# Performance work log

Measured on AMD Instinct MI355X. Metric: run time of the kernel, lower is better.

Reference implementation:

```python
import jax, jax.numpy as jnp
import numpy as np

B, T, D, H = 64, 512, 512, 128

def swish(x):
    return x * jax.nn.sigmoid(x)

def setup_inputs() -> dict:
    key = jax.random.key(0)
    ks = jax.random.split(key, 8)
    X = jax.random.normal(ks[0], (B, T, D), dtype=jnp.float32)
    # strictly-upper-triangular random binary adjacency -> valid DAG
    adj = jax.random.bernoulli(ks[1], 0.3, (T, T)).astype(jnp.float32)
    dag = jnp.triu(adj, k=1)
    s = 1.0 / np.sqrt(D)
    Wk = jax.random.normal(ks[2], (H, D), dtype=jnp.float32) * s
    bk = jax.random.normal(ks[3], (H,), dtype=jnp.float32) * 0.01
    Wq = jax.random.normal(ks[4], (H, D), dtype=jnp.float32) * s
    bq = jax.random.normal(ks[5], (H,), dtype=jnp.float32) * 0.01
    Wv = jax.random.normal(ks[6], (H, D), dtype=jnp.float32) * s
    bv = jax.random.normal(ks[7], (H,), dtype=jnp.float32) * 0.01
    return {"X": X, "dag": dag, "Wk": Wk, "bk": bk, "Wq": Wq, "bq": bq, "Wv": Wv, "bv": bv}

def reference(X, dag, Wk, bk, Wq, bq, Wv, bv):
    K = swish(jnp.einsum('btd,hd->bth', X, Wk) + bk)  # [B,T,H]
    Q = swish(jnp.einsum('btd,hd->bth', X, Wq) + bq)
    V = swish(jnp.einsum('btd,hd->bth', X, Wv) + bv)
    S_qk = jnp.einsum('bqh,bkh->bqk', Q, K) / jnp.sqrt(jnp.float32(H))  # [B,T,T]
    dagT = dag.T  # [T,T]
    Sprime = dagT * jnp.einsum('ij,bjk->bik', dagT, S_qk)  # [B,T,T]
    # masked_fill(Sprime == 0, -inf) then softmax; rows that are all -inf
    # would produce NaN in torch and are replaced by zeros -> do it nan-free.
    nz = Sprime != 0
    masked = jnp.where(nz, Sprime, -jnp.inf)
    row_valid = jnp.any(nz, axis=-1, keepdims=True)  # [B,T,1]
    masked_safe = jnp.where(row_valid, masked, 0.0)
    probs = jax.nn.softmax(masked_safe, axis=-1) * row_valid  # [B,T,T]
    Vprime = jnp.einsum('ij,bjh->bih', dagT, V)  # [B,T,H]
    O = jnp.einsum('bqk,bkh->bqh', probs, V) + Vprime
    return O
```

## Files before the change

kernel.cpp:

```cpp
#include <hip/hip_runtime.h>
#include <hip/hip_bf16.h>

#define Bn 64
#define Tn 512
#define Dn 512
#define Hn 128
#define BT (Bn*Tn)

typedef unsigned short u16;
typedef unsigned long long u64;
typedef __attribute__((ext_vector_type(8))) short bf16x8;
typedef __attribute__((ext_vector_type(4))) float f32x4;

__device__ __forceinline__ u16 f2bf(float f) {
  union { float f; unsigned u; } v; v.f = f;
  unsigned r = (v.u + 0x7FFFu + ((v.u >> 16) & 1u)) >> 16;
  return (u16)r;
}

__device__ __forceinline__ bf16x8 pack8(float4 a, float4 b) {
  bf16x8 o;
  o[0] = (short)f2bf(a.x); o[1] = (short)f2bf(a.y);
  o[2] = (short)f2bf(a.z); o[3] = (short)f2bf(a.w);
  o[4] = (short)f2bf(b.x); o[5] = (short)f2bf(b.y);
  o[6] = (short)f2bf(b.z); o[7] = (short)f2bf(b.w);
  return o;
}

__device__ __forceinline__ void gload16(const void* g, void* lds) {
  __builtin_amdgcn_global_load_lds(
      (const __attribute__((address_space(1))) unsigned int*)g,
      (__attribute__((address_space(3))) unsigned int*)lds, 16, 0, 0);
}

__global__ __launch_bounds__(256) void conv_w3(const float4* __restrict__ Wk,
                                               const float4* __restrict__ Wq,
                                               const float4* __restrict__ Wv,
                                               ushort4* __restrict__ out) {
  int idx = blockIdx.x * 256 + threadIdx.x;
  int which = idx >> 14, j = idx & 16383;
  const float4* src = (which == 0) ? Wk : (which == 1) ? Wq : Wv;
  float4 v = src[j];
  ushort4 o; o.x = f2bf(v.x); o.y = f2bf(v.y); o.z = f2bf(v.z); o.w = f2bf(v.w);
  out[idx] = o;
}

__global__ __launch_bounds__(256) void dag_tr(const float* __restrict__ dag,
                                              u16* __restrict__ dagT,
                                              u64* __restrict__ bits) {
  __shared__ float s[64][65];
  int bx = blockIdx.x & 7, by = blockIdx.x >> 3;
  int r0 = by * 64, c0 = bx * 64;
  int t = threadIdx.x;
  int c4 = t & 15, rr = t >> 4;
#pragma unroll
  for (int q = 0; q < 4; ++q) {
    int r = rr + q * 16;
    float4 v = *(const float4*)&dag[(size_t)(r0 + r) * Tn + c0 + c4 * 4];
    s[c4 * 4 + 0][r] = v.x; s[c4 * 4 + 1][r] = v.y;
    s[c4 * 4 + 2][r] = v.z; s[c4 * 4 + 3][r] = v.w;
  }
  __syncthreads();
#pragma unroll
  for (int q = 0; q < 4; ++q) {
    int il = rr + q * 16;
    ushort4 o;
    u64 b4 = 0;
#pragma unroll
    for (int r = 0; r < 4; ++r) {
      float v = s[il][c4 * 4 + r];
      ((u16*)&o)[r] = f2bf(v);
      b4 |= (u64)(v != 0.f) << (c4 * 4 + r);
    }
    *(ushort4*)&dagT[(size_t)(c0 + il) * Tn + r0 + c4 * 4] = o;
    b4 |= __shfl_xor(b4, 1, 64);
    b4 |= __shfl_xor(b4, 2, 64);
    b4 |= __shfl_xor(b4, 4, 64);
    b4 |= __shfl_xor(b4, 8, 64);
    if (c4 == 0) bits[(size_t)(c0 + il) * 8 + (r0 >> 6)] = b4;
  }
}

__global__ __launch_bounds__(256, 2) void qkv3(
    const float* __restrict__ X, const u16* __restrict__ Wcat,
    const float* __restrict__ bk, const float* __restrict__ bq,
    const float* __restrict__ bv,
    u16* __restrict__ Kb, u16* __restrict__ QT, u16* __restrict__ VT) {
  __shared__ u16 sm[28672];
  int m0 = blockIdx.x * 64;
  int tid = threadIdx.x, lane = tid & 63, wave = tid >> 6;
  int col0 = lane & 15, rg = lane >> 4, kcb = rg * 16;
  int swl = (col0 & 7) << 4;
  int xrow = tid >> 2, xcq = tid & 3;
  f32x4 acc[3][4][2] = {};
  const char* Wb = (const char*)Wcat;
  char* smb = (char*)sm;

  for (int kt = 0; kt < Dn; kt += 64) {
    {
      const float4* src = (const float4*)(X + (size_t)(m0 + xrow) * Dn + kt + xcq * 16);
      float4 a0 = src[0], a1 = src[1], a2 = src[2], a3 = src[3];
      int sw = (xrow & 7) << 4;
      *(bf16x8*)(smb + xrow * 128 + ((xcq * 32) ^ sw)) = pack8(a0, a1);
      *(bf16x8*)(smb + xrow * 128 + ((xcq * 32 + 16) ^ sw)) = pack8(a2, a3);
    }
#pragma unroll
    for (int q = 0; q < 12; ++q) {
      int c2 = wave * 12 + q;
      int which = c2 >> 4, idx = c2 & 15;
      int flat = idx * 1024 + lane * 16;
      int row = flat >> 7, colb = flat & 127;
      int sw = (row & 7) << 4;
      gload16(Wb + (size_t)which * 131072 + (size_t)row * 1024 + (kt << 1) + (colb ^ sw),
              smb + 8192 + which * 16384 + idx * 1024);
    }
    __syncthreads();
    bf16x8 af[4][2];
#pragma unroll
    for (int m = 0; m < 4; ++m)
#pragma unroll
      for (int kk = 0; kk < 2; ++kk)
        af[m][kk] = *(const bf16x8*)(smb + (m * 16 + col0) * 128 + ((kk * 64 + kcb) ^ swl));
#pragma unroll
    for (int which = 0; which < 3; ++which) {
      bf16x8 bfr[2][2];
#pragma unroll
      for (int n = 0; n < 2; ++n)
#pragma unroll
        for (int kk = 0; kk < 2; ++kk)
          bfr[n][kk] = *(const bf16x8*)(smb + 8192 + which * 16384 +
                                        (wave * 32 + n * 16 + col0) * 128 + ((kk * 64 + kcb) ^ swl));
#pragma unroll
      for (int kk = 0; kk < 2; ++kk)
#pragma unroll
        for (int m = 0; m < 4; ++m)
#pragma unroll
          for (int n = 0; n < 2; ++n)
            acc[which][m][n] = __builtin_amdgcn_mfma_f32_16x16x32_bf16(
                af[m][kk], bfr[n][kk], acc[which][m][n], 0, 0, 0);
    }
    __syncthreads();
  }

  {
#pragma unroll
    for (int n = 0; n < 2; ++n) {
      int nl = wave * 32 + n * 16 + col0;
      float bs = bk[nl];
#pragma unroll
      for (int m = 0; m < 4; ++m)
#pragma unroll
        for (int r = 0; r < 4; ++r) {
          int tl = m * 16 + rg * 4 + r;
          float x = acc[0][m][n][r] + bs;
          *(u16*)(smb + tl * 256 + ((nl * 2) ^ ((tl & 7) << 4))) = f2bf(x / (1.f + __expf(-x)));
        }
    }
    __syncthreads();
#pragma unroll
    for (int p = 0; p < 4; ++p) {
      int c = p * 256 + tid;
      int t = c >> 4, c16 = c & 15;
      bf16x8 v = *(const bf16x8*)(smb + t * 256 + ((c16 * 16) ^ ((t & 7) << 4)));
      *(bf16x8*)&Kb[(size_t)(m0 + t) * Hn + c16 * 8] = v;
    }
  }
  int bb = m0 >> 9, tt0 = m0 & (Tn - 1);
#pragma unroll
  for (int which = 1; which < 3; ++which) {
    const float* bias = (which == 1) ? bq : bv;
    u16* dst = (which == 1) ? QT : VT;
    __syncthreads();
#pragma unroll
    for (int n = 0; n < 2; ++n) {
      int nl = wave * 32 + n * 16 + col0;
      float bs = bias[nl];
#pragma unroll
      for (int m = 0; m < 4; ++m)
#pragma unroll
        for (int r = 0; r < 4; ++r) {
          int tl = m * 16 + rg * 4 + r;
          float x = acc[which][m][n][r] + bs;
          *(u16*)(smb + nl * 128 + ((tl * 2) ^ ((nl & 7) << 4))) = f2bf(x / (1.f + __expf(-x)));
        }
    }
    __syncthreads();
#pragma unroll
    for (int p = 0; p < 4; ++p) {
      int c = p * 256 + tid;
      int h = c >> 3, c8 = c & 7;
      bf16x8 v = *(const bf16x8*)(smb + h * 128 + ((c8 * 16) ^ ((h & 7) << 4)));
      *(bf16x8*)&dst[((size_t)bb * Hn + h) * Tn + tt0 + c8 * 8] = v;
    }
  }
}

__global__ __launch_bounds__(256, 2) void dattn(
    const u16* __restrict__ dagT, const u16* __restrict__ QT,
    const u16* __restrict__ VT, const u16* __restrict__ Kb,
    const u64* __restrict__ dbits, float* __restrict__ O) {
  __shared__ char smA[65536];
  __shared__ u16 smQ2[8192];

  int bid = blockIdx.x;
  int xcd = bid & 7, rst = bid >> 3;
  int bx = rst & 7, b = (rst >> 3) * 8 + xcd;
  int m0 = bx * 64;
  int tid = threadIdx.x, lane = tid & 63, wave = tid >> 6;
  int col0 = lane & 15, g = lane >> 4;
  int swl = (col0 & 7) << 4;

  const char* Ab = (const char*)(dagT + (size_t)m0 * Tn);
  const char* Qb = (const char*)(QT + (size_t)b * Hn * Tn);
  const char* Vb = (const char*)(VT + (size_t)b * Hn * Tn);
  const char* Kb0 = (const char*)(Kb + (size_t)b * Tn * Hn);

  f32x4 accq[4][2] = {};
  f32x4 accv[4][2] = {};
  for (int kt = 0; kt < Tn; kt += 64) {
#pragma unroll
    for (int q = 0; q < 2; ++q) {
      int ch = wave * 2 + q;
      int flat = ch * 1024 + lane * 16;
      int row = flat >> 7, colb = flat & 127;
      int sw = (row & 7) << 4;
      gload16(Ab + (size_t)row * 1024 + kt * 2 + (colb ^ sw), smA + ch * 1024);
    }
#pragma unroll
    for (int q = 0; q < 4; ++q) {
      int ch = wave * 4 + q;
      int flat = ch * 1024 + lane * 16;
      int row = flat >> 7, colb = flat & 127;
      int sw = (row & 7) << 4;
      gload16(Qb + (size_t)row * 1024 + kt * 2 + (colb ^ sw), smA + 8192 + ch * 1024);
      gload16(Vb + (size_t)row * 1024 + kt * 2 + (colb ^ sw), smA + 24576 + ch * 1024);
    }
    __syncthreads();
    bf16x8 af[4][2], fq[2][2], fv[2][2];
#pragma unroll
    for (int m = 0; m < 4; ++m)
#pragma unroll
      for (int kk = 0; kk < 2; ++kk)
        af[m][kk] = *(const bf16x8*)(smA + (m * 16 + col0) * 128 + ((kk * 64 + g * 16) ^ swl));
#pragma unroll
    for (int n = 0; n < 2; ++n)
#pragma unroll
      for (int kk = 0; kk < 2; ++kk) {
        fq[n][kk] = *(const bf16x8*)(smA + 8192 + (wave * 32 + n * 16 + col0) * 128 + ((kk * 64 + g * 16) ^ swl));
        fv[n][kk] = *(const bf16x8*)(smA + 24576 + (wave * 32 + n * 16 + col0) * 128 + ((kk * 64 + g * 16) ^ swl));
      }
#pragma unroll
    for (int kk = 0; kk < 2; ++kk)
#pragma unroll
      for (int m = 0; m < 4; ++m)
#pragma unroll
        for (int n = 0; n < 2; ++n) {
          accq[m][n] = __builtin_amdgcn_mfma_f32_16x16x32_bf16(af[m][kk], fq[n][kk], accq[m][n], 0, 0, 0);
          accv[m][n] = __builtin_amdgcn_mfma_f32_16x16x32_bf16(af[m][kk], fv[n][kk], accv[m][n], 0, 0, 0);
        }
    __syncthreads();
  }

  const float scale = 0.08838834764831845f;
#pragma unroll
  for (int m = 0; m < 4; ++m)
#pragma unroll
    for (int n = 0; n < 2; ++n)
#pragma unroll
      for (int r = 0; r < 4; ++r) {
        int q = m * 16 + g * 4 + r;
        int h = wave * 32 + n * 16 + col0;
        *(u16*)((char*)smQ2 + q * 256 + ((h * 2) ^ ((q & 7) << 4))) = f2bf(accq[m][n][r] * scale);
      }

#define STAGE_K(c_, buf_)                                                      \
  {                                                                            \
    _Pragma("unroll")                                                          \
    for (int q = 0; q < 8; ++q) {                                              \
      int ch = wave * 8 + q;                                                   \
      int flat = ch * 1024 + lane * 16;                                        \
      int row = flat >> 8, colb = flat & 255;                                  \
      gload16(Kb0 + (size_t)((c_) * 128 + row) * 256 + (colb ^ ((row & 7) << 4)), \
              smA + (buf_) * 32768 + ch * 1024);                               \
    }                                                                          \
  }

  STAGE_K(0, 0);
  __syncthreads();

  int qrow = wave * 16 + col0;
  bf16x8 bq[4];
#pragma unroll
  for (int kk = 0; kk < 4; ++kk)
    bq[kk] = *(const bf16x8*)((char*)smQ2 + qrow * 256 + ((kk * 64 + g * 16) ^ ((qrow & 7) << 4)));
  const u64* dbq = dbits + (size_t)(m0 + qrow) * 8;
  u64 md[8];
#pragma unroll
  for (int w = 0; w < 8; ++w) md[w] = dbq[w];

  f32x4 sa[32] = {};
#pragma unroll
  for (int c = 0; c < 4; ++c) {
    if (c < 3) STAGE_K(c + 1, (c + 1) & 1);
    const char* kb = smA + (c & 1) * 32768;
#pragma unroll
    for (int t = 0; t < 8; ++t)
#pragma unroll
      for (int kk = 0; kk < 4; ++kk) {
        bf16x8 ak = *(const bf16x8*)(kb + (t * 16 + col0) * 256 + ((kk * 64 + g * 16) ^ swl));
        sa[c * 8 + t] = __builtin_amdgcn_mfma_f32_16x16x32_bf16(ak, bq[kk], sa[c * 8 + t], 0, 0, 0);
      }
    if (c < 3) __syncthreads();
  }

  float mx = -INFINITY;
#pragma unroll
  for (int t = 0; t < 32; ++t)
#pragma unroll
    for (int r = 0; r < 4; ++r) {
      int k = t * 16 + g * 4 + r;
      float v = ((md[k >> 6] >> (k & 63)) & 1) ? sa[t][r] : -INFINITY;
      sa[t][r] = v;
      mx = fmaxf(mx, v);
    }
  mx = fmaxf(mx, __shfl_xor(mx, 16, 64));
  mx = fmaxf(mx, __shfl_xor(mx, 32, 64));
  float mm = (mx == -INFINITY) ? 0.f : mx;

  ushort4 pk[32];
  float s = 0.f;
#pragma unroll
  for (int t = 0; t < 32; ++t) {
    ushort4 p;
#pragma unroll
    for (int r = 0; r < 4; ++r) {
      float v = sa[t][r];
      float e = (v == -INFINITY) ? 0.f : __expf(v - mm);
      s += e;
      ((u16*)&p)[r] = f2bf(e);
    }
    pk[t] = p;
  }
  s += __shfl_xor(s, 16, 64);
  s += __shfl_xor(s, 32, 64);
  float* linv = (float*)smQ2;
  if (g == 0) linv[qrow] = (s > 0.f) ? (1.f / s) : 0.f;

  char* smP = smA;
  f32x4 acco[4][2] = {};
  int sww = (qrow & 7) << 4;

#pragma unroll
  for (int c = 0; c < 4; ++c) {
    __syncthreads();
#pragma unroll
    for (int tt = 0; tt < 8; ++tt)
      *(ushort4*)(smP + qrow * 256 + ((tt * 32 + g * 8) ^ sww)) = pk[c * 8 + tt];
    __syncthreads();

#pragma unroll
    for (int kk = 0; kk < 4; ++kk) {
      bf16x8 pa[4], vb[2];
#pragma unroll
      for (int m = 0; m < 4; ++m) {
        int row = m * 16 + col0;
        pa[m] = *(const bf16x8*)(smP + row * 256 + ((kk * 64 + g * 16) ^ ((row & 7) << 4)));
      }
#pragma unroll
      for (int n = 0; n < 2; ++n)
        vb[n] = *(const bf16x8*)(Vb + (size_t)(wave * 32 + n * 16 + col0) * 1024 + c * 256 + kk * 64 + g * 16);
#pragma unroll
      for (int m = 0; m < 4; ++m)
#pragma unroll
        for (int n = 0; n < 2; ++n)
          acco[m][n] = __builtin_amdgcn_mfma_f32_16x16x32_bf16(pa[m], vb[n], acco[m][n], 0, 0, 0);
    }
  }

#pragma unroll
  for (int m = 0; m < 4; ++m)
#pragma unroll
    for (int r = 0; r < 4; ++r) {
      int ql = m * 16 + g * 4 + r;
      float inv = linv[ql];
      int i = m0 + ql;
#pragma unroll
      for (int n = 0; n < 2; ++n) {
        int h = wave * 32 + n * 16 + col0;
        O[((size_t)b * Tn + i) * Hn + h] = acco[m][n][r] * inv + accv[m][n][r];
      }
    }
#undef STAGE_K
}

extern "C" void kernel_launch(void* const* d_in, const int* in_sizes, int n_in,
                              void* d_out, int out_size, void* d_ws, size_t ws_size,
                              hipStream_t stream) {
  const float* X   = (const float*)d_in[0];
  const float* dag = (const float*)d_in[1];
  const float* Wk  = (const float*)d_in[2];
  const float* bk  = (const float*)d_in[3];
  const float* Wq  = (const float*)d_in[4];
  const float* bq  = (const float*)d_in[5];
  const float* Wv  = (const float*)d_in[6];
  const float* bv  = (const float*)d_in[7];
  float* O = (float*)d_out;

  char* ws = (char*)d_ws;
  u16* Wcat = (u16*)(ws);
  u16* dagT = (u16*)(ws + 393216);
  u64* dbits= (u64*)(ws + 917504);
  u16* Kb   = (u16*)(ws + 950272);
  u16* QT   = (u16*)(ws + 9338880);
  u16* VT   = (u16*)(ws + 17727488);

  conv_w3<<<192, 256, 0, stream>>>((const float4*)Wk, (const float4*)Wq,
                                   (const float4*)Wv, (ushort4*)Wcat);
  dag_tr<<<64, 256, 0, stream>>>(dag, dagT, dbits);

  qkv3<<<BT / 64, 256, 0, stream>>>(X, Wcat, bk, bq, bv, Kb, QT, VT);
  dattn<<<512, 256, 0, stream>>>(dagT, QT, VT, Kb, dbits, O);
}
```

Measured before the change: 79.49 us.

## Fold Vprime into PV accumulation and prefetch X in QKV kernel

The attention kernel no longer computes dagT·V in its first loop with separate V staging and accumulators. Instead it normalizes the probabilities before packing them to bf16 and adds a second MFMA per tile that multiplies dagT rows, read straight from global memory, by the same V fragments, so O accumulates P·V + dagT·V in one accumulator. This removes the V shared-memory staging, the extra accumulator registers and the per-row inverse lookup in the epilogue. In exchange it adds uncached-style global fragment reads of dagT in the inner loop. The QKV kernel also software-prefetches the next X tile into registers so the global load overlaps the MFMA work.

```diff
diff --git a/kernel.cpp b/kernel.cpp
--- a/kernel.cpp
+++ b/kernel.cpp
@@ -96,14 +96,21 @@
   const char* Wb = (const char*)Wcat;
   char* smb = (char*)sm;
 
+#define LOAD_X(kt_)                                                             \
+  {                                                                             \
+    const float4* s_ = (const float4*)(X + (size_t)(m0 + xrow) * Dn + (kt_) + xcq * 16); \
+    xa0 = s_[0]; xa1 = s_[1]; xa2 = s_[2]; xa3 = s_[3];                         \
+  }
+
+  float4 xa0, xa1, xa2, xa3;
+  LOAD_X(0);
   for (int kt = 0; kt < Dn; kt += 64) {
     {
-      const float4* src = (const float4*)(X + (size_t)(m0 + xrow) * Dn + kt + xcq * 16);
-      float4 a0 = src[0], a1 = src[1], a2 = src[2], a3 = src[3];
       int sw = (xrow & 7) << 4;
-      *(bf16x8*)(smb + xrow * 128 + ((xcq * 32) ^ sw)) = pack8(a0, a1);
-      *(bf16x8*)(smb + xrow * 128 + ((xcq * 32 + 16) ^ sw)) = pack8(a2, a3);
-    }
+      *(bf16x8*)(smb + xrow * 128 + ((xcq * 32) ^ sw)) = pack8(xa0, xa1);
+      *(bf16x8*)(smb + xrow * 128 + ((xcq * 32 + 16) ^ sw)) = pack8(xa2, xa3);
+    }
+    if (kt + 64 < Dn) LOAD_X(kt + 64);
 #pragma unroll
     for (int q = 0; q < 12; ++q) {
       int c2 = wave * 12 + q;
@@ -141,6 +148,7 @@
     }
     __syncthreads();
   }
+#undef LOAD_X
 
   {
 #pragma unroll
@@ -216,7 +224,6 @@
   const char* Kb0 = (const char*)(Kb + (size_t)b * Tn * Hn);
 
   f32x4 accq[4][2] = {};
-  f32x4 accv[4][2] = {};
   for (int kt = 0; kt < Tn; kt += 64) {
 #pragma unroll
     for (int q = 0; q < 2; ++q) {
@@ -233,10 +240,9 @@
       int row = flat >> 7, colb = flat & 127;
       int sw = (row & 7) << 4;
       gload16(Qb + (size_t)row * 1024 + kt * 2 + (colb ^ sw), smA + 8192 + ch * 1024);
-      gload16(Vb + (size_t)row * 1024 + kt * 2 + (colb ^ sw), smA + 24576 + ch * 1024);
-    }
-    __syncthreads();
-    bf16x8 af[4][2], fq[2][2], fv[2][2];
+    }
+    __syncthreads();
+    bf16x8 af[4][2], fq[2][2];
 #pragma unroll
     for (int m = 0; m < 4; ++m)
 #pragma unroll
@@ -245,19 +251,15 @@
 #pragma unroll
     for (int n = 0; n < 2; ++n)
 #pragma unroll
-      for (int kk = 0; kk < 2; ++kk) {
+      for (int kk = 0; kk < 2; ++kk)
         fq[n][kk] = *(const bf16x8*)(smA + 8192 + (wave * 32 + n * 16 + col0) * 128 + ((kk * 64 + g * 16) ^ swl));
-        fv[n][kk] = *(const bf16x8*)(smA + 24576 + (wave * 32 + n * 16 + col0) * 128 + ((kk * 64 + g * 16) ^ swl));
-      }
 #pragma unroll
     for (int kk = 0; kk < 2; ++kk)
 #pragma unroll
       for (int m = 0; m < 4; ++m)
 #pragma unroll
-        for (int n = 0; n < 2; ++n) {
+        for (int n = 0; n < 2; ++n)
           accq[m][n] = __builtin_amdgcn_mfma_f32_16x16x32_bf16(af[m][kk], fq[n][kk], accq[m][n], 0, 0, 0);
-          accv[m][n] = __builtin_amdgcn_mfma_f32_16x16x32_bf16(af[m][kk], fv[n][kk], accv[m][n], 0, 0, 0);
-        }
     __syncthreads();
   }
 
@@ -327,24 +329,28 @@
   mx = fmaxf(mx, __shfl_xor(mx, 32, 64));
   float mm = (mx == -INFINITY) ? 0.f : mx;
 
-  ushort4 pk[32];
+  float ev[32][4];
   float s = 0.f;
 #pragma unroll
-  for (int t = 0; t < 32; ++t) {
-    ushort4 p;
+  for (int t = 0; t < 32; ++t)
 #pragma unroll
     for (int r = 0; r < 4; ++r) {
       float v = sa[t][r];
       float e = (v == -INFINITY) ? 0.f : __expf(v - mm);
+      ev[t][r] = e;
       s += e;
-      ((u16*)&p)[r] = f2bf(e);
-    }
-    pk[t] = p;
-  }
+    }
   s += __shfl_xor(s, 16, 64);
   s += __shfl_xor(s, 32, 64);
-  float* linv = (float*)smQ2;
-  if (g == 0) linv[qrow] = (s > 0.f) ? (1.f / s) : 0.f;
+  float inv = (s > 0.f) ? (1.f / s) : 0.f;
+  ushort4 pk[32];
+#pragma unroll
+  for (int t = 0; t < 32; ++t) {
+    ushort4 p;
+#pragma unroll
+    for (int r = 0; r < 4; ++r) ((u16*)&p)[r] = f2bf(ev[t][r] * inv);
+    pk[t] = p;
+  }
 
   char* smP = smA;
   f32x4 acco[4][2] = {};
@@ -360,11 +366,12 @@
 
 #pragma unroll
     for (int kk = 0; kk < 4; ++kk) {
-      bf16x8 pa[4], vb[2];
+      bf16x8 pa[4], da[4], vb[2];
 #pragma unroll
       for (int m = 0; m < 4; ++m) {
         int row = m * 16 + col0;
         pa[m] = *(const bf16x8*)(smP + row * 256 + ((kk * 64 + g * 16) ^ ((row & 7) << 4)));
+        da[m] = *(const bf16x8*)(Ab + (size_t)row * 1024 + c * 256 + kk * 64 + g * 16);
       }
 #pragma unroll
       for (int n = 0; n < 2; ++n)
@@ -372,8 +379,10 @@
 #pragma unroll
       for (int m = 0; m < 4; ++m)
 #pragma unroll
-        for (int n = 0; n < 2; ++n)
+        for (int n = 0; n < 2; ++n) {
           acco[m][n] = __builtin_amdgcn_mfma_f32_16x16x32_bf16(pa[m], vb[n], acco[m][n], 0, 0, 0);
+          acco[m][n] = __builtin_amdgcn_mfma_f32_16x16x32_bf16(da[m], vb[n], acco[m][n], 0, 0, 0);
+        }
     }
   }
 
@@ -381,13 +390,11 @@
   for (int m = 0; m < 4; ++m)
 #pragma unroll
     for (int r = 0; r < 4; ++r) {
-      int ql = m * 16 + g * 4 + r;
-      float inv = linv[ql];
-      int i = m0 + ql;
+      int i = m0 + m * 16 + g * 4 + r;
 #pragma unroll
       for (int n = 0; n < 2; ++n) {
         int h = wave * 32 + n * 16 + col0;
-        O[((size_t)b * Tn + i) * Hn + h] = acco[m][n][r] * inv + accv[m][n][r];
+        O[((size_t)b * Tn + i) * Hn + h] = acco[m][n][r];
       }
     }
 #undef STAGE_K
```

After: 79.62 us. No clear change (+0.2%).
